# Performance work log

Hardware: AMD Instinct MI355X
Metric: run time of the kernel (lower is better)

Reference implementation:

```python
import jax, jax.numpy as jnp
import numpy as np

N_NODES = 100000
N_EDGES = 3200000
IN_DIM, HID, OUT_DIM = 128, 64, 32
N_LAYERS = 3


def setup_inputs() -> dict:
    key = jax.random.key(0)
    ks = jax.random.split(key, 10)
    x = jax.random.normal(ks[0], (N_NODES, IN_DIM), dtype=jnp.float32)
    edge_index = jax.random.randint(ks[1], (2, N_EDGES), 0, N_NODES, dtype=jnp.int64)
    edge_weight = jax.random.uniform(ks[2], (N_EDGES,), dtype=jnp.float32)
    s_in = 1.0 / np.sqrt(IN_DIM)
    s_h = 1.0 / np.sqrt(HID)
    W_in = jax.random.uniform(ks[3], (IN_DIM, HID), jnp.float32, -s_in, s_in)
    b_in = jax.random.uniform(ks[4], (HID,), jnp.float32, -s_in, s_in)
    W_g = jax.random.uniform(ks[5], (N_LAYERS, HID, HID), jnp.float32, -s_h, s_h)
    b_g = jax.random.uniform(ks[6], (N_LAYERS, HID), jnp.float32, -s_h, s_h)
    W_out = jax.random.uniform(ks[7], (HID, OUT_DIM), jnp.float32, -s_h, s_h)
    b_out = jax.random.uniform(ks[8], (OUT_DIM,), jnp.float32, -s_h, s_h)
    return {"x": x, "edge_index": edge_index, "edge_weight": edge_weight,
            "W_in": W_in, "b_in": b_in, "W_g": W_g, "b_g": b_g,
            "W_out": W_out, "b_out": b_out}


def reference(x, edge_index, edge_weight, W_in, b_in, W_g, b_g, W_out, b_out):
    # input projection: [N, IN_DIM] -> [N, HID]
    h = x @ W_in + b_in
    src = edge_index[0]
    dst = edge_index[1]
    num_nodes = h.shape[0]
    for l in range(N_LAYERS):
        # per-edge message: gather source features, scale by edge weight
        msg = h[src] * edge_weight[:, None]          # [E, HID]
        agg = jax.ops.segment_sum(msg, dst, num_segments=num_nodes)  # [N, HID]
        h = jax.nn.relu((h + agg) @ W_g[l] + b_g[l])
    return h @ W_out + b_out
```

## Files before the change

### kernel.cpp

```cpp
#include <hip/hip_runtime.h>
#include <hip/hip_bf16.h>
#include <hip/hip_fp16.h>

#define N_NODES 100000
#define IN_DIM 128
#define HID 64
#define OUT_DIM 32
#define BUCK 128
#define NB 782
#define CAP 5120
#define AST 68
#define CHUNK 8192
#define NBIN 512

typedef float floatx2 __attribute__((ext_vector_type(2)));
typedef short bf16x8 __attribute__((ext_vector_type(8)));
typedef float f32x4 __attribute__((ext_vector_type(4)));

__device__ __forceinline__ unsigned int pack4_fp8(float f0, float f1, float f2, float f3) {
    int u = __builtin_amdgcn_cvt_pk_fp8_f32(f0, f1, 0, false);
    u     = __builtin_amdgcn_cvt_pk_fp8_f32(f2, f3, u, true);
    return (unsigned int)u;
}

__device__ __forceinline__ unsigned short f2bf(float f) {
    unsigned int u = __float_as_uint(f);
    return (unsigned short)((u + 0x7FFFu + ((u >> 16) & 1u)) >> 16);
}

__global__ __launch_bounds__(512) void k_part(const int* __restrict__ src,
                                              const int* __restrict__ dst,
                                              const float* __restrict__ ew,
                                              int* __restrict__ bcur,
                                              unsigned int* __restrict__ ed, int E) {
    __shared__ int cnt[NB];
    __shared__ int lscan[NB];
    __shared__ int base[NB];
    __shared__ unsigned int stage[CHUNK];
    const int tid = threadIdx.x;
    const int lo = blockIdx.x * CHUNK;
    const int hi = min(E, lo + CHUNK);

    for (int i = tid; i < NB; i += 512) cnt[i] = 0;
    __syncthreads();
    for (int e = lo + tid; e < hi; e += 512)
        atomicAdd(&cnt[dst[e] >> 7], 1);
    __syncthreads();
    {
        const int i0 = tid, i1 = tid + 512;
        if (i0 < NB) lscan[i0] = cnt[i0];
        if (i1 < NB) lscan[i1] = cnt[i1];
        __syncthreads();
        for (int d = 1; d < 1024; d <<= 1) {
            int v0 = 0, v1 = 0;
            if (i0 >= d && i0 < NB) v0 = lscan[i0 - d];
            if (i1 >= d && i1 < NB) v1 = lscan[i1 - d];
            __syncthreads();
            if (i0 < NB) lscan[i0] += v0;
            if (i1 < NB) lscan[i1] += v1;
            __syncthreads();
        }
    }
    for (int i = tid; i < NB; i += 512) {
        int c = cnt[i];
        lscan[i] -= c;
        base[i] = c ? atomicAdd(&bcur[i], c) : 0;
        cnt[i] = 0;
    }
    __syncthreads();
    for (int e = lo + tid; e < hi; e += 512) {
        int d  = dst[e];
        int bk = d >> 7;
        unsigned int q = (unsigned int)(ew[e] * 256.0f);
        if (q > 255u) q = 255u;
        int r = atomicAdd(&cnt[bk], 1);
        stage[lscan[bk] + r] = (unsigned int)src[e]
                               | ((unsigned int)(d & 127) << 17) | (q << 24);
    }
    __syncthreads();
    for (int b = tid; b < NB; b += 512) {
        int c = cnt[b];
        if (!c) continue;
        int room = CAP - base[b];
        int m = c < room ? c : (room > 0 ? room : 0);
        const unsigned int* s = &stage[lscan[b]];
        unsigned int* g = ed + (size_t)b * CAP + base[b];
        for (int i = 0; i < m; ++i) g[i] = s[i];
    }
}

__global__ __launch_bounds__(512) void k_sort(const unsigned int* __restrict__ ed,
                                              unsigned int* __restrict__ ed2,
                                              const int* __restrict__ bcur,
                                              int* __restrict__ off,
                                              int* __restrict__ endo) {
    __shared__ int cnt[NBIN];
    __shared__ int inc[NBIN];
    __shared__ int cur[NBIN];
    const int tid = threadIdx.x;
    const int bkt = blockIdx.x;
    const int b0 = bkt * CAP;
    const int b1 = b0 + min(bcur[bkt], CAP);

    cnt[tid] = 0;
    __syncthreads();
    for (int i = b0 + tid; i < b1; i += 512) {
        const unsigned int e = ed[i];
        const int key = (((e >> 17) & 127) << 2) | ((e >> 15) & 3);
        atomicAdd(&cnt[key], 1);
    }
    __syncthreads();
    inc[tid] = cnt[tid];
    __syncthreads();
    for (int d = 1; d < NBIN; d <<= 1) {
        int v = 0;
        if (tid >= d) v = inc[tid - d];
        __syncthreads();
        inc[tid] += v;
        __syncthreads();
    }
    cur[tid] = inc[tid] - cnt[tid];
    if (tid < BUCK) {
        const int n = bkt * BUCK + tid;
        if (n < N_NODES) {
            off[n]  = b0 + inc[tid * 4] - cnt[tid * 4];
            endo[n] = b0 + inc[tid * 4 + 3];
        }
    }
    __syncthreads();
    for (int i = b0 + tid; i < b1; i += 512) {
        const unsigned int e = ed[i];
        const int key = (((e >> 17) & 127) << 2) | ((e >> 15) & 3);
        const int p = atomicAdd(&cur[key], 1);
        ed2[b0 + p] = e;
    }
}

__global__ __launch_bounds__(256) void k_wc(const float* __restrict__ W_in,
                                            const float* __restrict__ b_in,
                                            const float* __restrict__ Wg0,
                                            unsigned short* __restrict__ wct,
                                            float* __restrict__ bc) {
    __shared__ float sWg[HID * HID];
    __shared__ float sWi[16 * HID];
    const int tid = threadIdx.x;
    const int k0 = blockIdx.x * 16;
    for (int i = tid; i < HID * HID; i += 256) sWg[i] = Wg0[i];
    for (int i = tid; i < 16 * HID; i += 256) sWi[i] = W_in[k0 * HID + i];
    __syncthreads();
    const int kr = tid >> 4;
    const int jb = (tid & 15) * 4;
    float c0 = 0.f, c1 = 0.f, c2 = 0.f, c3 = 0.f;
#pragma unroll 4
    for (int m = 0; m < HID; ++m) {
        const float a = sWi[kr * HID + m];
        const float4 wv = *(const float4*)&sWg[m * HID + jb];
        c0 = fmaf(a, wv.x, c0); c1 = fmaf(a, wv.y, c1);
        c2 = fmaf(a, wv.z, c2); c3 = fmaf(a, wv.w, c3);
    }
    const int k = k0 + kr;
    wct[(size_t)(jb + 0) * IN_DIM + k] = f2bf(c0);
    wct[(size_t)(jb + 1) * IN_DIM + k] = f2bf(c1);
    wct[(size_t)(jb + 2) * IN_DIM + k] = f2bf(c2);
    wct[(size_t)(jb + 3) * IN_DIM + k] = f2bf(c3);
    if (blockIdx.x == 0 && tid < HID) {
        float s = 0.f;
        for (int m = 0; m < HID; ++m) s = fmaf(b_in[m], sWg[m * HID + tid], s);
        bc[tid] = s;
    }
}

__global__ __launch_bounds__(256) void k_proj0(const float* __restrict__ x,
                                               const unsigned short* __restrict__ wct,
                                               const float* __restrict__ bc,
                                               unsigned int* __restrict__ g0) {
    __shared__ float sH[4][32][76];
    const int tid = threadIdx.x;
    const int w = tid >> 6, lane = tid & 63;
    const int lr = lane & 15, lg = lane >> 4;
    const int nb0 = blockIdx.x * 128 + w * 32;

    bf16x8 B[4][4];
#pragma unroll
    for (int j = 0; j < 4; ++j)
#pragma unroll
        for (int c = 0; c < 4; ++c)
            B[j][c] = *(const bf16x8*)(wct + (16 * j + lr) * IN_DIM + 32 * c + 8 * lg);

    f32x4 acc[2][4];
#pragma unroll
    for (int mt = 0; mt < 2; ++mt)
#pragma unroll
        for (int j = 0; j < 4; ++j)
            acc[mt][j] = (f32x4){0.f, 0.f, 0.f, 0.f};

#pragma unroll
    for (int mt = 0; mt < 2; ++mt) {
        int n = nb0 + mt * 16 + lr;
        if (n >= N_NODES) n = N_NODES - 1;
        const float* xr = x + (size_t)n * IN_DIM + 8 * lg;
        bf16x8 A[4];
#pragma unroll
        for (int c = 0; c < 4; ++c) {
            const float4 lo = *(const float4*)(xr + 32 * c);
            const float4 hi = *(const float4*)(xr + 32 * c + 4);
            bf16x8 a;
            a[0] = (short)f2bf(lo.x); a[1] = (short)f2bf(lo.y);
            a[2] = (short)f2bf(lo.z); a[3] = (short)f2bf(lo.w);
            a[4] = (short)f2bf(hi.x); a[5] = (short)f2bf(hi.y);
            a[6] = (short)f2bf(hi.z); a[7] = (short)f2bf(hi.w);
            A[c] = a;
        }
#pragma unroll
        for (int j = 0; j < 4; ++j)
#pragma unroll
            for (int c = 0; c < 4; ++c)
                acc[mt][j] = __builtin_amdgcn_mfma_f32_16x16x32_bf16(
                    A[c], B[j][c], acc[mt][j], 0, 0, 0);
    }

#pragma unroll
    for (int j = 0; j < 4; ++j) {
        const float bj = bc[16 * j + lr];
#pragma unroll
        for (int mt = 0; mt < 2; ++mt)
#pragma unroll
            for (int r = 0; r < 4; ++r)
                sH[w][mt * 16 + 4 * lg + r][16 * j + lr] = acc[mt][j][r] + bj;
    }
    __syncthreads();

#pragma unroll
    for (int i = 0; i < 8; ++i) {
        const int idx = lane + 64 * i;
        const int nl = idx >> 4, jq = idx & 15;
        const int n = nb0 + nl;
        if (n < N_NODES) {
            const float4 v = *(const float4*)&sH[w][nl][jq * 4];
            g0[(size_t)n * 16 + jq] = pack4_fp8(v.x, v.y, v.z, v.w);
        }
    }
}

#define ROW(p)  (gp[((size_t)((p) & 0x1FFFFu)) * 8])
#define WT(p)   (((float)((p) >> 24) + 0.5f) * 0.00390625f)
#define ACC(p, v) do { const float w_ = WT(p); const floatx2 w2 = {w_, w_};     \
        A01 += w2 * __builtin_amdgcn_cvt_pk_f32_fp8((v).x, false);              \
        A23 += w2 * __builtin_amdgcn_cvt_pk_f32_fp8((v).x, true);               \
        A45 += w2 * __builtin_amdgcn_cvt_pk_f32_fp8((v).y, false);              \
        A67 += w2 * __builtin_amdgcn_cvt_pk_f32_fp8((v).y, true); } while (0)

#define AGG_GATHER_BODY                                                        \
    floatx2 A01 = {0.f, 0.f}, A23 = {0.f, 0.f},                                \
            A45 = {0.f, 0.f}, A67 = {0.f, 0.f};                                \
    if (valid) {                                                               \
        uint2 sv = gp[(size_t)n * 8];                                          \
        A01 = __builtin_amdgcn_cvt_pk_f32_fp8(sv.x, false);                    \
        A23 = __builtin_amdgcn_cvt_pk_f32_fp8(sv.x, true);                     \
        A45 = __builtin_amdgcn_cvt_pk_f32_fp8(sv.y, false);                    \
        A67 = __builtin_amdgcn_cvt_pk_f32_fp8(sv.y, true);                     \
        int i = off[n];                                                        \
        const int i1 = endo[n];                                                \
        if (i + 4 <= i1) {                                                     \
            unsigned int p0 = ed2[i], p1 = ed2[i+1], p2 = ed2[i+2], p3 = ed2[i+3]; \
            uint2 v0 = ROW(p0), v1 = ROW(p1), v2 = ROW(p2), v3 = ROW(p3);      \
            i += 4;                                                            \
            for (; i + 4 <= i1; i += 4) {                                      \
                unsigned int q0 = ed2[i], q1 = ed2[i+1], q2 = ed2[i+2], q3 = ed2[i+3]; \
                uint2 w0 = ROW(q0), w1 = ROW(q1), w2 = ROW(q2), w3 = ROW(q3);  \
                ACC(p0, v0); ACC(p1, v1); ACC(p2, v2); ACC(p3, v3);            \
                p0 = q0; p1 = q1; p2 = q2; p3 = q3;                            \
                v0 = w0; v1 = w1; v2 = w2; v3 = w3;                            \
            }                                                                  \
            ACC(p0, v0); ACC(p1, v1); ACC(p2, v2); ACC(p3, v3);                \
        }                                                                      \
        for (; i < i1; ++i) { unsigned int p = ed2[i]; uint2 v = ROW(p); ACC(p, v); } \
    }                                                                          \
    const float a0 = A01.x, a1 = A01.y, a2 = A23.x, a3 = A23.y,                \
                a4 = A45.x, a5 = A45.y, a6 = A67.x, a7 = A67.y;

__global__ __launch_bounds__(512) void k_agg_mid(
        const unsigned int* __restrict__ g_in,
        unsigned int* __restrict__ g_out,
        const unsigned int* __restrict__ ed2,
        const int* __restrict__ off, const int* __restrict__ endo,
        const float* __restrict__ bg, const float* __restrict__ Wnext) {
    __shared__ float sHT[HID][AST];
    __shared__ float sW[HID * HID];
    const int tid = threadIdx.x;
    const int grp = tid >> 3, l8 = tid & 7;
    const int n = blockIdx.x * 64 + grp;
    const bool valid = (n < N_NODES);
    const uint2* gp = (const uint2*)g_in + l8;

    for (int i = tid; i < HID * HID; i += 512) sW[i] = Wnext[i];

    AGG_GATHER_BODY

    const float4 bA = *(const float4*)(bg + l8 * 8);
    const float4 bB = *(const float4*)(bg + l8 * 8 + 4);
    const int f0 = l8 * 8;
    sHT[f0 + 0][grp] = valid ? fmaxf(a0 + bA.x, 0.f) : 0.f;
    sHT[f0 + 1][grp] = valid ? fmaxf(a1 + bA.y, 0.f) : 0.f;
    sHT[f0 + 2][grp] = valid ? fmaxf(a2 + bA.z, 0.f) : 0.f;
    sHT[f0 + 3][grp] = valid ? fmaxf(a3 + bA.w, 0.f) : 0.f;
    sHT[f0 + 4][grp] = valid ? fmaxf(a4 + bB.x, 0.f) : 0.f;
    sHT[f0 + 5][grp] = valid ? fmaxf(a5 + bB.y, 0.f) : 0.f;
    sHT[f0 + 6][grp] = valid ? fmaxf(a6 + bB.z, 0.f) : 0.f;
    sHT[f0 + 7][grp] = valid ? fmaxf(a7 + bB.w, 0.f) : 0.f;
    __syncthreads();

    const int npr = tid >> 4;
    const int jq  = tid & 15;
    const int jb  = jq * 4;
    float c0[4] = {0.f, 0.f, 0.f, 0.f};
    float c1[4] = {0.f, 0.f, 0.f, 0.f};
#pragma unroll 4
    for (int k = 0; k < HID; ++k) {
        const float2 a = *(const float2*)&sHT[k][npr * 2];
        const float4 w = *(const float4*)&sW[k * HID + jb];
        c0[0] = fmaf(a.x, w.x, c0[0]); c0[1] = fmaf(a.x, w.y, c0[1]);
        c0[2] = fmaf(a.x, w.z, c0[2]); c0[3] = fmaf(a.x, w.w, c0[3]);
        c1[0] = fmaf(a.y, w.x, c1[0]); c1[1] = fmaf(a.y, w.y, c1[1]);
        c1[2] = fmaf(a.y, w.z, c1[2]); c1[3] = fmaf(a.y, w.w, c1[3]);
    }
    const int nbase = blockIdx.x * 64 + npr * 2;
    if (nbase < N_NODES)
        g_out[(size_t)nbase * 16 + jq] = pack4_fp8(c0[0], c0[1], c0[2], c0[3]);
    if (nbase + 1 < N_NODES)
        g_out[(size_t)(nbase + 1) * 16 + jq] = pack4_fp8(c1[0], c1[1], c1[2], c1[3]);
}

__global__ __launch_bounds__(512) void k_agg_out(
        const unsigned int* __restrict__ g_in,
        float* __restrict__ out,
        const unsigned int* __restrict__ ed2,
        const int* __restrict__ off, const int* __restrict__ endo,
        const float* __restrict__ bg, const float* __restrict__ W_out,
        const float* __restrict__ b_out) {
    __shared__ float sHT[HID][AST];
    __shared__ float sW[HID * OUT_DIM];
    const int tid = threadIdx.x;
    const int grp = tid >> 3, l8 = tid & 7;
    const int n = blockIdx.x * 64 + grp;
    const bool valid = (n < N_NODES);
    const uint2* gp = (const uint2*)g_in + l8;

    for (int i = tid; i < HID * OUT_DIM; i += 512) sW[i] = W_out[i];

    AGG_GATHER_BODY

    const float4 bA = *(const float4*)(bg + l8 * 8);
    const float4 bB = *(const float4*)(bg + l8 * 8 + 4);
    const int f0 = l8 * 8;
    sHT[f0 + 0][grp] = valid ? fmaxf(a0 + bA.x, 0.f) : 0.f;
    sHT[f0 + 1][grp] = valid ? fmaxf(a1 + bA.y, 0.f) : 0.f;
    sHT[f0 + 2][grp] = valid ? fmaxf(a2 + bA.z, 0.f) : 0.f;
    sHT[f0 + 3][grp] = valid ? fmaxf(a3 + bA.w, 0.f) : 0.f;
    sHT[f0 + 4][grp] = valid ? fmaxf(a4 + bB.x, 0.f) : 0.f;
    sHT[f0 + 5][grp] = valid ? fmaxf(a5 + bB.y, 0.f) : 0.f;
    sHT[f0 + 6][grp] = valid ? fmaxf(a6 + bB.z, 0.f) : 0.f;
    sHT[f0 + 7][grp] = valid ? fmaxf(a7 + bB.w, 0.f) : 0.f;
    __syncthreads();

    const int node = tid >> 3;
    const int jb   = (tid & 7) * 4;
    const float4 bo = *(const float4*)(b_out + jb);
    float c4[4] = {bo.x, bo.y, bo.z, bo.w};
#pragma unroll 4
    for (int k = 0; k < HID; ++k) {
        const float a = sHT[k][node];
        const float4 w = *(const float4*)&sW[k * OUT_DIM + jb];
        c4[0] = fmaf(a, w.x, c4[0]); c4[1] = fmaf(a, w.y, c4[1]);
        c4[2] = fmaf(a, w.z, c4[2]); c4[3] = fmaf(a, w.w, c4[3]);
    }
    const int n2 = blockIdx.x * 64 + node;
    if (n2 < N_NODES)
        *(float4*)(out + (size_t)n2 * OUT_DIM + jb) =
            make_float4(c4[0], c4[1], c4[2], c4[3]);
}

#undef ROW
#undef WT
#undef ACC
#undef AGG_GATHER_BODY

extern "C" void kernel_launch(void* const* d_in, const int* in_sizes, int n_in,
                              void* d_out, int out_size, void* d_ws, size_t ws_size,
                              hipStream_t stream) {
    const float* x     = (const float*)d_in[0];
    const int*   ei    = (const int*)d_in[1];
    const float* ew    = (const float*)d_in[2];
    const float* W_in  = (const float*)d_in[3];
    const float* b_in  = (const float*)d_in[4];
    const float* W_g   = (const float*)d_in[5];
    const float* b_g   = (const float*)d_in[6];
    const float* W_out = (const float*)d_in[7];
    const float* b_out = (const float*)d_in[8];
    float* out = (float*)d_out;

    const int E = in_sizes[2];
    const int* src = ei;
    const int* dst = ei + E;

    char* ws = (char*)d_ws;
    unsigned int* ed  = (unsigned int*)ws;
    unsigned int* ed2 = ed + (size_t)NB * CAP;
    unsigned int* gA  = ed2 + (size_t)NB * CAP;
    unsigned int* gB  = gA + (size_t)N_NODES * 16;
    int* misc = (int*)(gB + (size_t)N_NODES * 16);
    int* off  = misc;
    int* endo = misc + 100032;
    int* bcur = misc + 200064;

    const int nparts = (E + CHUNK - 1) / CHUNK;

    unsigned short* wct = (unsigned short*)ed;
    float* bcv = (float*)(ed + 4096);

    k_wc<<<8, 256, 0, stream>>>(W_in, b_in, W_g, wct, bcv);
    k_proj0<<<(N_NODES + 127) / 128, 256, 0, stream>>>(x, wct, bcv, gA);

    hipMemsetAsync(bcur, 0, NB * sizeof(int), stream);
    k_part<<<nparts, 512, 0, stream>>>(src, dst, ew, bcur, ed, E);
    k_sort<<<NB, 512, 0, stream>>>(ed, ed2, bcur, off, endo);

    k_agg_mid<<<(N_NODES + 63) / 64, 512, 0, stream>>>(
        gA, gB, ed2, off, endo, b_g + 0 * HID, W_g + 1 * HID * HID);
    k_agg_mid<<<(N_NODES + 63) / 64, 512, 0, stream>>>(
        gB, gA, ed2, off, endo, b_g + 1 * HID, W_g + 2 * HID * HID);
    k_agg_out<<<(N_NODES + 63) / 64, 512, 0, stream>>>(
        gA, out, ed2, off, endo, b_g + 2 * HID, W_out, b_out);
}
```

Before: 338.5 us.

## Fuse edge partitioning and input projection into one heterogeneous kernel launch

```diff
diff --git a/kernel.cpp b/kernel.cpp
--- a/kernel.cpp
+++ b/kernel.cpp
@@ -12,6 +12,7 @@
 #define AST 68
 #define CHUNK 8192
 #define NBIN 512
+#define FSMEM 42176
 
 typedef float floatx2 __attribute__((ext_vector_type(2)));
 typedef short bf16x8 __attribute__((ext_vector_type(8)));
@@ -28,64 +29,121 @@
     return (unsigned short)((u + 0x7FFFu + ((u >> 16) & 1u)) >> 16);
 }
 
-__global__ __launch_bounds__(512) void k_part(const int* __restrict__ src,
-                                              const int* __restrict__ dst,
-                                              const float* __restrict__ ew,
-                                              int* __restrict__ bcur,
-                                              unsigned int* __restrict__ ed, int E) {
-    __shared__ int cnt[NB];
-    __shared__ int lscan[NB];
-    __shared__ int base[NB];
-    __shared__ unsigned int stage[CHUNK];
+__global__ __launch_bounds__(512, 4) void k_fused(
+        const int* __restrict__ src, const int* __restrict__ dst,
+        const float* __restrict__ ew, int* __restrict__ bcur,
+        unsigned int* __restrict__ ed, int E, int npart,
+        const float* __restrict__ x, const unsigned short* __restrict__ wct,
+        const float* __restrict__ bc, unsigned int* __restrict__ g0) {
+    __shared__ __align__(16) char smem[FSMEM];
     const int tid = threadIdx.x;
-    const int lo = blockIdx.x * CHUNK;
-    const int hi = min(E, lo + CHUNK);
-
-    for (int i = tid; i < NB; i += 512) cnt[i] = 0;
-    __syncthreads();
-    for (int e = lo + tid; e < hi; e += 512)
-        atomicAdd(&cnt[dst[e] >> 7], 1);
-    __syncthreads();
-    {
-        const int i0 = tid, i1 = tid + 512;
-        if (i0 < NB) lscan[i0] = cnt[i0];
-        if (i1 < NB) lscan[i1] = cnt[i1];
-        __syncthreads();
-        for (int d = 1; d < 1024; d <<= 1) {
-            int v0 = 0, v1 = 0;
-            if (i0 >= d && i0 < NB) v0 = lscan[i0 - d];
-            if (i1 >= d && i1 < NB) v1 = lscan[i1 - d];
+
+    if ((int)blockIdx.x < npart) {
+        int* cnt   = (int*)smem;
+        int* lscan = cnt + NB;
+        int* base  = lscan + NB;
+        unsigned int* stage = (unsigned int*)(base + NB);
+        const int lo = blockIdx.x * CHUNK;
+        const int hi = min(E, lo + CHUNK);
+
+        for (int i = tid; i < NB; i += 512) cnt[i] = 0;
+        __syncthreads();
+        for (int e = lo + tid; e < hi; e += 512)
+            atomicAdd(&cnt[dst[e] >> 7], 1);
+        __syncthreads();
+        {
+            const int i0 = tid, i1 = tid + 512;
+            if (i0 < NB) lscan[i0] = cnt[i0];
+            if (i1 < NB) lscan[i1] = cnt[i1];
             __syncthreads();
-            if (i0 < NB) lscan[i0] += v0;
-            if (i1 < NB) lscan[i1] += v1;
-            __syncthreads();
-        }
-    }
-    for (int i = tid; i < NB; i += 512) {
-        int c = cnt[i];
-        lscan[i] -= c;
-        base[i] = c ? atomicAdd(&bcur[i], c) : 0;
-        cnt[i] = 0;
-    }
-    __syncthreads();
-    for (int e = lo + tid; e < hi; e += 512) {
-        int d  = dst[e];
-        int bk = d >> 7;
-        unsigned int q = (unsigned int)(ew[e] * 256.0f);
-        if (q > 255u) q = 255u;
-        int r = atomicAdd(&cnt[bk], 1);
-        stage[lscan[bk] + r] = (unsigned int)src[e]
-                               | ((unsigned int)(d & 127) << 17) | (q << 24);
-    }
-    __syncthreads();
-    for (int b = tid; b < NB; b += 512) {
-        int c = cnt[b];
-        if (!c) continue;
-        int room = CAP - base[b];
-        int m = c < room ? c : (room > 0 ? room : 0);
-        const unsigned int* s = &stage[lscan[b]];
-        unsigned int* g = ed + (size_t)b * CAP + base[b];
-        for (int i = 0; i < m; ++i) g[i] = s[i];
+            for (int d = 1; d < 1024; d <<= 1) {
+                int v0 = 0, v1 = 0;
+                if (i0 >= d && i0 < NB) v0 = lscan[i0 - d];
+                if (i1 >= d && i1 < NB) v1 = lscan[i1 - d];
+                __syncthreads();
+                if (i0 < NB) lscan[i0] += v0;
+                if (i1 < NB) lscan[i1] += v1;
+                __syncthreads();
+            }
+        }
+        for (int i = tid; i < NB; i += 512) {
+            int c = cnt[i];
+            lscan[i] -= c;
+            base[i] = c ? atomicAdd(&bcur[i], c) : 0;
+            cnt[i] = 0;
+        }
+        __syncthreads();
+        for (int e = lo + tid; e < hi; e += 512) {
+            int d  = dst[e];
+            int bk = d >> 7;
+            unsigned int q = (unsigned int)(ew[e] * 256.0f);
+            if (q > 255u) q = 255u;
+            int r = atomicAdd(&cnt[bk], 1);
+            stage[lscan[bk] + r] = (unsigned int)src[e]
+                                   | ((unsigned int)(d & 127) << 17) | (q << 24);
+        }
+        __syncthreads();
+        for (int b = tid; b < NB; b += 512) {
+            int c = cnt[b];
+            if (!c) continue;
+            int room = CAP - base[b];
+            int m = c < room ? c : (room > 0 ? room : 0);
+            const unsigned int* s = &stage[lscan[b]];
+            unsigned int* g = ed + (size_t)b * CAP + base[b];
+            for (int i = 0; i < m; ++i) g[i] = s[i];
+        }
+    } else {
+        float* sHall = (float*)smem;
+        const int w = tid >> 6, lane = tid & 63;
+        const int lr = lane & 15, lg = lane >> 4;
+        const int nb0 = ((int)blockIdx.x - npart) * 128 + w * 16;
+        float* sH = sHall + w * (16 * 68);
+
+        f32x4 acc[4];
+#pragma unroll
+        for (int j = 0; j < 4; ++j) acc[j] = (f32x4){0.f, 0.f, 0.f, 0.f};
+
+        int n = nb0 + lr;
+        if (n >= N_NODES) n = N_NODES - 1;
+        const float* xr = x + (size_t)n * IN_DIM + 8 * lg;
+        bf16x8 A[4];
+#pragma unroll
+        for (int c = 0; c < 4; ++c) {
+            const float4 lo4 = *(const float4*)(xr + 32 * c);
+            const float4 hi4 = *(const float4*)(xr + 32 * c + 4);
+            bf16x8 a;
+            a[0] = (short)f2bf(lo4.x); a[1] = (short)f2bf(lo4.y);
+            a[2] = (short)f2bf(lo4.z); a[3] = (short)f2bf(lo4.w);
+            a[4] = (short)f2bf(hi4.x); a[5] = (short)f2bf(hi4.y);
+            a[6] = (short)f2bf(hi4.z); a[7] = (short)f2bf(hi4.w);
+            A[c] = a;
+        }
+#pragma unroll
+        for (int j = 0; j < 4; ++j) {
+#pragma unroll
+            for (int c = 0; c < 4; ++c) {
+                const bf16x8 B = *(const bf16x8*)(wct + (16 * j + lr) * IN_DIM
+                                                  + 32 * c + 8 * lg);
+                acc[j] = __builtin_amdgcn_mfma_f32_16x16x32_bf16(A[c], B, acc[j], 0, 0, 0);
+            }
+        }
+#pragma unroll
+        for (int j = 0; j < 4; ++j) {
+            const float bj = bc[16 * j + lr];
+#pragma unroll
+            for (int r = 0; r < 4; ++r)
+                sH[(4 * lg + r) * 68 + 16 * j + lr] = acc[j][r] + bj;
+        }
+#pragma unroll
+        for (int i = 0; i < 4; ++i) {
+            const int idx = lane + 64 * i;
+            const int nl = idx >> 4, jq = idx & 15;
+            const int n2 = nb0 + nl;
+            if (n2 < N_NODES) {
+                const float4 v = *(const float4*)&sH[nl * 68 + jq * 4];
+                g0[(size_t)n2 * 16 + jq] = pack4_fp8(v.x, v.y, v.z, v.w);
+            }
+        }
     }
 }
 
@@ -167,78 +225,6 @@
         float s = 0.f;
         for (int m = 0; m < HID; ++m) s = fmaf(b_in[m], sWg[m * HID + tid], s);
         bc[tid] = s;
-    }
-}
-
-__global__ __launch_bounds__(256) void k_proj0(const float* __restrict__ x,
-                                               const unsigned short* __restrict__ wct,
-                                               const float* __restrict__ bc,
-                                               unsigned int* __restrict__ g0) {
-    __shared__ float sH[4][32][76];
-    const int tid = threadIdx.x;
-    const int w = tid >> 6, lane = tid & 63;
-    const int lr = lane & 15, lg = lane >> 4;
-    const int nb0 = blockIdx.x * 128 + w * 32;
-
-    bf16x8 B[4][4];
-#pragma unroll
-    for (int j = 0; j < 4; ++j)
-#pragma unroll
-        for (int c = 0; c < 4; ++c)
-            B[j][c] = *(const bf16x8*)(wct + (16 * j + lr) * IN_DIM + 32 * c + 8 * lg);
-
-    f32x4 acc[2][4];
-#pragma unroll
-    for (int mt = 0; mt < 2; ++mt)
-#pragma unroll
-        for (int j = 0; j < 4; ++j)
-            acc[mt][j] = (f32x4){0.f, 0.f, 0.f, 0.f};
-
-#pragma unroll
-    for (int mt = 0; mt < 2; ++mt) {
-        int n = nb0 + mt * 16 + lr;
-        if (n >= N_NODES) n = N_NODES - 1;
-        const float* xr = x + (size_t)n * IN_DIM + 8 * lg;
-        bf16x8 A[4];
-#pragma unroll
-        for (int c = 0; c < 4; ++c) {
-            const float4 lo = *(const float4*)(xr + 32 * c);
-            const float4 hi = *(const float4*)(xr + 32 * c + 4);
-            bf16x8 a;
-            a[0] = (short)f2bf(lo.x); a[1] = (short)f2bf(lo.y);
-            a[2] = (short)f2bf(lo.z); a[3] = (short)f2bf(lo.w);
-            a[4] = (short)f2bf(hi.x); a[5] = (short)f2bf(hi.y);
-            a[6] = (short)f2bf(hi.z); a[7] = (short)f2bf(hi.w);
-            A[c] = a;
-        }
-#pragma unroll
-        for (int j = 0; j < 4; ++j)
-#pragma unroll
-            for (int c = 0; c < 4; ++c)
-                acc[mt][j] = __builtin_amdgcn_mfma_f32_16x16x32_bf16(
-                    A[c], B[j][c], acc[mt][j], 0, 0, 0);
-    }
-
-#pragma unroll
-    for (int j = 0; j < 4; ++j) {
-        const float bj = bc[16 * j + lr];
-#pragma unroll
-        for (int mt = 0; mt < 2; ++mt)
-#pragma unroll
-            for (int r = 0; r < 4; ++r)
-                sH[w][mt * 16 + 4 * lg + r][16 * j + lr] = acc[mt][j][r] + bj;
-    }
-    __syncthreads();
-
-#pragma unroll
-    for (int i = 0; i < 8; ++i) {
-        const int idx = lane + 64 * i;
-        const int nl = idx >> 4, jq = idx & 15;
-        const int n = nb0 + nl;
-        if (n < N_NODES) {
-            const float4 v = *(const float4*)&sH[w][nl][jq * 4];
-            g0[(size_t)n * 16 + jq] = pack4_fp8(v.x, v.y, v.z, v.w);
-        }
     }
 }
 
@@ -412,17 +398,18 @@
     int* off  = misc;
     int* endo = misc + 100032;
     int* bcur = misc + 200064;
+    unsigned short* wct = (unsigned short*)(misc + 201088);
+    float* bcv = (float*)(wct + IN_DIM * HID);
 
     const int nparts = (E + CHUNK - 1) / CHUNK;
-
-    unsigned short* wct = (unsigned short*)ed;
-    float* bcv = (float*)(ed + 4096);
+    const int nproj  = (N_NODES + 127) / 128;
 
     k_wc<<<8, 256, 0, stream>>>(W_in, b_in, W_g, wct, bcv);
-    k_proj0<<<(N_NODES + 127) / 128, 256, 0, stream>>>(x, wct, bcv, gA);
-
     hipMemsetAsync(bcur, 0, NB * sizeof(int), stream);
-    k_part<<<nparts, 512, 0, stream>>>(src, dst, ew, bcur, ed, E);
+
+    k_fused<<<nparts + nproj, 512, 0, stream>>>(
+        src, dst, ew, bcur, ed, E, nparts, x, wct, bcv, gA);
+
     k_sort<<<NB, 512, 0, stream>>>(ed, ed2, bcur, off, endo);
 
     k_agg_mid<<<(N_NODES + 63) / 64, 512, 0, stream>>>(
```

Result: faster. 325.7 us (-3.8%).
